# Kernel tuning notes

Hardware: AMD Instinct MI355X
Metric: run time of the kernel (lower is better)

Reference implementation:

```python
import jax, jax.numpy as jnp
import numpy as np

D_K = 64

def setup_inputs() -> dict:
    key = jax.random.key(0)
    kq, kk, kv, km = jax.random.split(key, 4)
    B, H, S, D = 2, 16, 2048, D_K
    q = jax.random.normal(kq, (B, H, S, D), dtype=jnp.float32)
    k = jax.random.normal(kk, (B, H, S, D), dtype=jnp.float32)
    v = jax.random.normal(kv, (B, H, S, D), dtype=jnp.float32)
    atten_mask = jax.random.bernoulli(km, 0.1, (B, H, S, S))  # True = masked out
    return {"q": q, "k": k, "v": v, "atten_mask": atten_mask}

def reference(q, k, v, atten_mask):
    # score = q @ k^T / sqrt(d_k)  -> [B, H, S, S]
    score = jnp.einsum("bhqd,bhkd->bhqk", q, k) / np.sqrt(D_K).astype(np.float32)
    score = jnp.where(atten_mask, jnp.float32(-1e9), score)
    attn = jax.nn.softmax(score, axis=-1)
    return attn  # original module stops before the AV matmul (v unused)
```

## Files before the change

kernel.cpp:

```cpp
#include <hip/hip_runtime.h>

typedef _Float16 f16x8 __attribute__((ext_vector_type(8)));
typedef _Float16 f16x4 __attribute__((ext_vector_type(4)));
typedef float    f32x4 __attribute__((ext_vector_type(4)));
typedef int      i32x4 __attribute__((ext_vector_type(4)));

#define S_LEN 2048
#define D_KH  64
#define NBH   32
#define QTILE 16
#define NBLK  (NBH * (S_LEN / QTILE))
#define THREADS 512
#define QK_ELEMS (NBH * S_LEN * D_KH)

__device__ __forceinline__ f16x8 cvt8(const float4 a, const float4 b) {
  f16x8 r;
  r[0] = (_Float16)a.x; r[1] = (_Float16)a.y;
  r[2] = (_Float16)a.z; r[3] = (_Float16)a.w;
  r[4] = (_Float16)b.x; r[5] = (_Float16)b.y;
  r[6] = (_Float16)b.z; r[7] = (_Float16)b.w;
  return r;
}

__global__ __launch_bounds__(256) void cvt_qk_kernel(
    const float* __restrict__ q, const float* __restrict__ kmat,
    _Float16* __restrict__ qh, _Float16* __restrict__ kh) {
  const long long idx = ((long long)blockIdx.x * 256 + threadIdx.x) * 8;
  float4 q0 = *(const float4*)(q + idx);
  float4 q1 = *(const float4*)(q + idx + 4);
  const float s = 0.125f;
  q0.x *= s; q0.y *= s; q0.z *= s; q0.w *= s;
  q1.x *= s; q1.y *= s; q1.z *= s; q1.w *= s;
  *(f16x8*)(qh + idx) = cvt8(q0, q1);
  const float4 k0 = *(const float4*)(kmat + idx);
  const float4 k1 = *(const float4*)(kmat + idx + 4);
  *(f16x8*)(kh + idx) = cvt8(k0, k1);
}

__device__ __forceinline__ void softmax_row_lds(
    const _Float16* __restrict__ srow, const i32x4* __restrict__ m,
    const int physx, const int l, float* __restrict__ op) {
  float mx = -3.0e38f;
  #pragma unroll
  for (int i = 0; i < 8; ++i) {
    const int col = (i << 8) + (l << 2);
    const f16x4 h = *(const f16x4*)&srow[col ^ physx];
    mx = fmaxf(mx, m[i].x ? -1.0e9f : (float)h[0]);
    mx = fmaxf(mx, m[i].y ? -1.0e9f : (float)h[1]);
    mx = fmaxf(mx, m[i].z ? -1.0e9f : (float)h[2]);
    mx = fmaxf(mx, m[i].w ? -1.0e9f : (float)h[3]);
  }
  #pragma unroll
  for (int off = 32; off > 0; off >>= 1)
    mx = fmaxf(mx, __shfl_xor(mx, off, 64));
  float sum = 0.f;
  #pragma unroll
  for (int i = 0; i < 8; ++i) {
    const int col = (i << 8) + (l << 2);
    const f16x4 h = *(const f16x4*)&srow[col ^ physx];
    sum += __expf((m[i].x ? -1.0e9f : (float)h[0]) - mx);
    sum += __expf((m[i].y ? -1.0e9f : (float)h[1]) - mx);
    sum += __expf((m[i].z ? -1.0e9f : (float)h[2]) - mx);
    sum += __expf((m[i].w ? -1.0e9f : (float)h[3]) - mx);
  }
  #pragma unroll
  for (int off = 32; off > 0; off >>= 1)
    sum += __shfl_xor(sum, off, 64);
  const float inv = 1.0f / sum;
  #pragma unroll
  for (int i = 0; i < 8; ++i) {
    const int col = (i << 8) + (l << 2);
    const f16x4 h = *(const f16x4*)&srow[col ^ physx];
    f32x4 o = { __expf((m[i].x ? -1.0e9f : (float)h[0]) - mx) * inv,
                __expf((m[i].y ? -1.0e9f : (float)h[1]) - mx) * inv,
                __expf((m[i].z ? -1.0e9f : (float)h[2]) - mx) * inv,
                __expf((m[i].w ? -1.0e9f : (float)h[3]) - mx) * inv };
    __builtin_nontemporal_store(o, (f32x4*)(op + col));
  }
}

template <bool F16>
__global__ __launch_bounds__(THREADS, 4) void sdpa_probs_kernel(
    const float* __restrict__ qf, const float* __restrict__ kf,
    const _Float16* __restrict__ qh, const _Float16* __restrict__ kh,
    const int* __restrict__ mask, float* __restrict__ out) {
  const int bid = (int)blockIdx.x;
  const int nb  = (bid & 7) * (NBLK / 8) + (bid >> 3);
  const int bh  = nb >> 7;
  const int qt  = nb & 127;

  __shared__ _Float16 sc[QTILE][S_LEN];

  const int tid   = (int)threadIdx.x;
  const int w     = tid >> 6;
  const int l     = tid & 63;
  const int lo    = l & 15;
  const int g     = l >> 4;
  const int dbase = g << 3;

  const size_t qk_bh = (size_t)bh * S_LEN * D_KH;
  const size_t obh   = (size_t)bh * S_LEN * S_LEN;

  const int rowA = w << 1, rowB = rowA + 1;
  const size_t orowA = obh + (size_t)(qt * QTILE + rowA) * S_LEN;
  const size_t orowB = obh + (size_t)(qt * QTILE + rowB) * S_LEN;

  i32x4 mA[8], mB[8];
  {
    const int* mpA = mask + orowA + (l << 2);
    const int* mpB = mask + orowB + (l << 2);
    #pragma unroll
    for (int i = 0; i < 8; ++i) {
      mA[i] = __builtin_nontemporal_load((const i32x4*)(mpA + (i << 8)));
      mB[i] = __builtin_nontemporal_load((const i32x4*)(mpB + (i << 8)));
    }
  }

  f16x8 a0, a1;
  if constexpr (F16) {
    const _Float16* qp = qh + qk_bh + (size_t)(qt * QTILE + lo) * D_KH + dbase;
    a0 = *(const f16x8*)qp;
    a1 = *(const f16x8*)(qp + 32);
  } else {
    const float* qp = qf + qk_bh + (size_t)(qt * QTILE + lo) * D_KH;
    float4 t0 = *(const float4*)(qp + dbase);
    float4 t1 = *(const float4*)(qp + dbase + 4);
    float4 t2 = *(const float4*)(qp + dbase + 32);
    float4 t3 = *(const float4*)(qp + dbase + 36);
    const float s = 0.125f;
    t0.x *= s; t0.y *= s; t0.z *= s; t0.w *= s;
    t1.x *= s; t1.y *= s; t1.z *= s; t1.w *= s;
    t2.x *= s; t2.y *= s; t2.z *= s; t2.w *= s;
    t3.x *= s; t3.y *= s; t3.z *= s; t3.w *= s;
    a0 = cvt8(t0, t1);
    a1 = cvt8(t2, t3);
  }

  #pragma unroll 2
  for (int kt = 0; kt < 16; ++kt) {
    const int kcol = (w << 8) + (kt << 4) + lo;
    f16x8 b0, b1;
    if constexpr (F16) {
      const _Float16* kp = kh + qk_bh + (size_t)kcol * D_KH + dbase;
      b0 = *(const f16x8*)kp;
      b1 = *(const f16x8*)(kp + 32);
    } else {
      const float* kp = kf + qk_bh + (size_t)kcol * D_KH + dbase;
      b0 = cvt8(*(const float4*)(kp), *(const float4*)(kp + 4));
      b1 = cvt8(*(const float4*)(kp + 32), *(const float4*)(kp + 36));
    }
    f32x4 acc = {0.f, 0.f, 0.f, 0.f};
    acc = __builtin_amdgcn_mfma_f32_16x16x32_f16(a0, b0, acc, 0, 0, 0);
    acc = __builtin_amdgcn_mfma_f32_16x16x32_f16(a1, b1, acc, 0, 0, 0);
    const int phys = kcol ^ (g << 4);
    #pragma unroll
    for (int r = 0; r < 4; ++r)
      sc[(g << 2) + r][phys] = (_Float16)acc[r];
  }

  #pragma unroll
  for (int i = 0; i < 8; ++i) asm volatile("" :: "v"(mA[i]), "v"(mB[i]));
  __syncthreads();

  const int physx = (w >> 1) << 4;
  softmax_row_lds(&sc[rowA][0], mA, physx, l, out + orowA);
  softmax_row_lds(&sc[rowB][0], mB, physx, l, out + orowB);
}

extern "C" void kernel_launch(void* const* d_in, const int* in_sizes, int n_in,
                              void* d_out, int out_size, void* d_ws, size_t ws_size,
                              hipStream_t stream) {
  const float* q    = (const float*)d_in[0];
  const float* kmat = (const float*)d_in[1];
  const int*   mask = (const int*)d_in[3];
  float*       out  = (float*)d_out;

  const size_t need = (size_t)QK_ELEMS * 2 * sizeof(_Float16);
  if (ws_size >= need) {
    _Float16* qh = (_Float16*)d_ws;
    _Float16* kh = qh + QK_ELEMS;
    cvt_qk_kernel<<<dim3(QK_ELEMS / 8 / 256), dim3(256), 0, stream>>>(q, kmat, qh, kh);
    sdpa_probs_kernel<true><<<dim3(NBLK), dim3(THREADS), 0, stream>>>(
        nullptr, nullptr, qh, kh, mask, out);
  } else {
    sdpa_probs_kernel<false><<<dim3(NBLK), dim3(THREADS), 0, stream>>>(
        q, kmat, nullptr, nullptr, mask, out);
  }
}
```

Before: 236.2 us.

## Persistent blocks loop over query tiles, prefetching next tile's mask

The grid shrinks to 512 persistent blocks, each looping over 8 query tiles instead of one tile per block. The mask rows for the next tile are loaded during the current tile's softmax, hiding mask load latency behind compute. The mask is also packed into a 32-bit bitfield per row so fewer registers stay live across the loop. Masked entries now skip the exp. This adds two barriers per tile and reduces the number of blocks available for latency hiding.

New measurement: 399.7 us. +69.2%, slower.

```diff
diff --git a/kernel.cpp b/kernel.cpp
--- a/kernel.cpp
+++ b/kernel.cpp
@@ -9,8 +9,9 @@
 #define D_KH  64
 #define NBH   32
 #define QTILE 16
-#define NBLK  (NBH * (S_LEN / QTILE))
 #define THREADS 512
+#define NBLOCKS 512
+#define NT 8
 #define QK_ELEMS (NBH * S_LEN * D_KH)
 
 __device__ __forceinline__ f16x8 cvt8(const float4 a, const float4 b) {
@@ -37,44 +38,47 @@
   *(f16x8*)(kh + idx) = cvt8(k0, k1);
 }
 
-__device__ __forceinline__ void softmax_row_lds(
-    const _Float16* __restrict__ srow, const i32x4* __restrict__ m,
-    const int physx, const int l, float* __restrict__ op) {
+__device__ __forceinline__ void softmax_row_packed(
+    const _Float16* __restrict__ srow, const unsigned pm, const int physx,
+    const int l, float* __restrict__ op) {
   float mx = -3.0e38f;
+  #pragma unroll
+  for (int i = 0; i < 8; ++i) {
+    const int off = (((i << 8) + (l << 2))) ^ physx;
+    const f16x4 h = *(const f16x4*)&srow[off];
+    const unsigned b = pm >> (4 * i);
+    mx = fmaxf(mx, (b & 1u) ? -1.0e9f : (float)h[0]);
+    mx = fmaxf(mx, (b & 2u) ? -1.0e9f : (float)h[1]);
+    mx = fmaxf(mx, (b & 4u) ? -1.0e9f : (float)h[2]);
+    mx = fmaxf(mx, (b & 8u) ? -1.0e9f : (float)h[3]);
+  }
+  #pragma unroll
+  for (int off = 32; off > 0; off >>= 1)
+    mx = fmaxf(mx, __shfl_xor(mx, off, 64));
+  float sum = 0.f;
+  #pragma unroll
+  for (int i = 0; i < 8; ++i) {
+    const int off = (((i << 8) + (l << 2))) ^ physx;
+    const f16x4 h = *(const f16x4*)&srow[off];
+    const unsigned b = pm >> (4 * i);
+    sum += (b & 1u) ? 0.f : __expf((float)h[0] - mx);
+    sum += (b & 2u) ? 0.f : __expf((float)h[1] - mx);
+    sum += (b & 4u) ? 0.f : __expf((float)h[2] - mx);
+    sum += (b & 8u) ? 0.f : __expf((float)h[3] - mx);
+  }
+  #pragma unroll
+  for (int off = 32; off > 0; off >>= 1)
+    sum += __shfl_xor(sum, off, 64);
+  const float inv = 1.0f / sum;
   #pragma unroll
   for (int i = 0; i < 8; ++i) {
     const int col = (i << 8) + (l << 2);
     const f16x4 h = *(const f16x4*)&srow[col ^ physx];
-    mx = fmaxf(mx, m[i].x ? -1.0e9f : (float)h[0]);
-    mx = fmaxf(mx, m[i].y ? -1.0e9f : (float)h[1]);
-    mx = fmaxf(mx, m[i].z ? -1.0e9f : (float)h[2]);
-    mx = fmaxf(mx, m[i].w ? -1.0e9f : (float)h[3]);
-  }
-  #pragma unroll
-  for (int off = 32; off > 0; off >>= 1)
-    mx = fmaxf(mx, __shfl_xor(mx, off, 64));
-  float sum = 0.f;
-  #pragma unroll
-  for (int i = 0; i < 8; ++i) {
-    const int col = (i << 8) + (l << 2);
-    const f16x4 h = *(const f16x4*)&srow[col ^ physx];
-    sum += __expf((m[i].x ? -1.0e9f : (float)h[0]) - mx);
-    sum += __expf((m[i].y ? -1.0e9f : (float)h[1]) - mx);
-    sum += __expf((m[i].z ? -1.0e9f : (float)h[2]) - mx);
-    sum += __expf((m[i].w ? -1.0e9f : (float)h[3]) - mx);
-  }
-  #pragma unroll
-  for (int off = 32; off > 0; off >>= 1)
-    sum += __shfl_xor(sum, off, 64);
-  const float inv = 1.0f / sum;
-  #pragma unroll
-  for (int i = 0; i < 8; ++i) {
-    const int col = (i << 8) + (l << 2);
-    const f16x4 h = *(const f16x4*)&srow[col ^ physx];
-    f32x4 o = { __expf((m[i].x ? -1.0e9f : (float)h[0]) - mx) * inv,
-                __expf((m[i].y ? -1.0e9f : (float)h[1]) - mx) * inv,
-                __expf((m[i].z ? -1.0e9f : (float)h[2]) - mx) * inv,
-                __expf((m[i].w ? -1.0e9f : (float)h[3]) - mx) * inv };
+    const unsigned b = pm >> (4 * i);
+    f32x4 o = { (b & 1u) ? 0.f : __expf((float)h[0] - mx) * inv,
+                (b & 2u) ? 0.f : __expf((float)h[1] - mx) * inv,
+                (b & 4u) ? 0.f : __expf((float)h[2] - mx) * inv,
+                (b & 8u) ? 0.f : __expf((float)h[3] - mx) * inv };
     __builtin_nontemporal_store(o, (f32x4*)(op + col));
   }
 }
@@ -85,9 +89,9 @@
     const _Float16* __restrict__ qh, const _Float16* __restrict__ kh,
     const int* __restrict__ mask, float* __restrict__ out) {
   const int bid = (int)blockIdx.x;
-  const int nb  = (bid & 7) * (NBLK / 8) + (bid >> 3);
-  const int bh  = nb >> 7;
-  const int qt  = nb & 127;
+  const int nb  = (bid & 7) * (NBLOCKS / 8) + (bid >> 3);
+  const int bh  = nb >> 4;
+  const int jb  = nb & 15;
 
   __shared__ _Float16 sc[QTILE][S_LEN];
 
@@ -101,70 +105,93 @@
   const size_t qk_bh = (size_t)bh * S_LEN * D_KH;
   const size_t obh   = (size_t)bh * S_LEN * S_LEN;
 
-  const int rowA = w << 1, rowB = rowA + 1;
-  const size_t orowA = obh + (size_t)(qt * QTILE + rowA) * S_LEN;
-  const size_t orowB = obh + (size_t)(qt * QTILE + rowB) * S_LEN;
-
-  i32x4 mA[8], mB[8];
-  {
-    const int* mpA = mask + orowA + (l << 2);
-    const int* mpB = mask + orowB + (l << 2);
+  const int rowA = w << 1, rowB = rowA | 1;
+  const int physx = (w >> 1) << 4;
+
+  i32x4 rawA[8], rawB[8];
+
+#define ISSUE_MASKS(qt_) do {                                                  \
+    const int* mpA_ = mask + obh + (size_t)((qt_) * QTILE + rowA) * S_LEN + (l << 2); \
+    const int* mpB_ = mask + obh + (size_t)((qt_) * QTILE + rowB) * S_LEN + (l << 2); \
+    _Pragma("unroll")                                                          \
+    for (int i_ = 0; i_ < 8; ++i_) {                                           \
+      rawA[i_] = __builtin_nontemporal_load((const i32x4*)(mpA_ + (i_ << 8))); \
+      rawB[i_] = __builtin_nontemporal_load((const i32x4*)(mpB_ + (i_ << 8))); \
+    }                                                                          \
+  } while (0)
+
+  ISSUE_MASKS(jb * NT);
+
+  for (int t = 0; t < NT; ++t) {
+    const int qt = jb * NT + t;
+
+    f16x8 a0, a1;
+    if constexpr (F16) {
+      const _Float16* qp = qh + qk_bh + (size_t)(qt * QTILE + lo) * D_KH + dbase;
+      a0 = *(const f16x8*)qp;
+      a1 = *(const f16x8*)(qp + 32);
+    } else {
+      const float* qp = qf + qk_bh + (size_t)(qt * QTILE + lo) * D_KH;
+      float4 t0 = *(const float4*)(qp + dbase);
+      float4 t1 = *(const float4*)(qp + dbase + 4);
+      float4 t2 = *(const float4*)(qp + dbase + 32);
+      float4 t3 = *(const float4*)(qp + dbase + 36);
+      const float s = 0.125f;
+      t0.x *= s; t0.y *= s; t0.z *= s; t0.w *= s;
+      t1.x *= s; t1.y *= s; t1.z *= s; t1.w *= s;
+      t2.x *= s; t2.y *= s; t2.z *= s; t2.w *= s;
+      t3.x *= s; t3.y *= s; t3.z *= s; t3.w *= s;
+      a0 = cvt8(t0, t1);
+      a1 = cvt8(t2, t3);
+    }
+
+    #pragma unroll 2
+    for (int kt = 0; kt < 16; ++kt) {
+      const int kcol = (w << 8) + (kt << 4) + lo;
+      f16x8 b0, b1;
+      if constexpr (F16) {
+        const _Float16* kp = kh + qk_bh + (size_t)kcol * D_KH + dbase;
+        b0 = *(const f16x8*)kp;
+        b1 = *(const f16x8*)(kp + 32);
+      } else {
+        const float* kp = kf + qk_bh + (size_t)kcol * D_KH + dbase;
+        b0 = cvt8(*(const float4*)(kp), *(const float4*)(kp + 4));
+        b1 = cvt8(*(const float4*)(kp + 32), *(const float4*)(kp + 36));
+      }
+      f32x4 acc = {0.f, 0.f, 0.f, 0.f};
+      acc = __builtin_amdgcn_mfma_f32_16x16x32_f16(a0, b0, acc, 0, 0, 0);
+      acc = __builtin_amdgcn_mfma_f32_16x16x32_f16(a1, b1, acc, 0, 0, 0);
+      const int phys = kcol ^ (g << 4);
+      #pragma unroll
+      for (int r = 0; r < 4; ++r)
+        sc[(g << 2) + r][phys] = (_Float16)acc[r];
+    }
+
+    unsigned pA = 0, pB = 0;
     #pragma unroll
     for (int i = 0; i < 8; ++i) {
-      mA[i] = __builtin_nontemporal_load((const i32x4*)(mpA + (i << 8)));
-      mB[i] = __builtin_nontemporal_load((const i32x4*)(mpB + (i << 8)));
+      pA |= ((rawA[i].x != 0 ? 1u : 0u) << (4 * i))
+          | ((rawA[i].y != 0 ? 1u : 0u) << (4 * i + 1))
+          | ((rawA[i].z != 0 ? 1u : 0u) << (4 * i + 2))
+          | ((rawA[i].w != 0 ? 1u : 0u) << (4 * i + 3));
+      pB |= ((rawB[i].x != 0 ? 1u : 0u) << (4 * i))
+          | ((rawB[i].y != 0 ? 1u : 0u) << (4 * i + 1))
+          | ((rawB[i].z != 0 ? 1u : 0u) << (4 * i + 2))
+          | ((rawB[i].w != 0 ? 1u : 0u) << (4 * i + 3));
     }
-  }
-
-  f16x8 a0, a1;
-  if constexpr (F16) {
-    const _Float16* qp = qh + qk_bh + (size_t)(qt * QTILE + lo) * D_KH + dbase;
-    a0 = *(const f16x8*)qp;
-    a1 = *(const f16x8*)(qp + 32);
-  } else {
-    const float* qp = qf + qk_bh + (size_t)(qt * QTILE + lo) * D_KH;
-    float4 t0 = *(const float4*)(qp + dbase);
-    float4 t1 = *(const float4*)(qp + dbase + 4);
-    float4 t2 = *(const float4*)(qp + dbase + 32);
-    float4 t3 = *(const float4*)(qp + dbase + 36);
-    const float s = 0.125f;
-    t0.x *= s; t0.y *= s; t0.z *= s; t0.w *= s;
-    t1.x *= s; t1.y *= s; t1.z *= s; t1.w *= s;
-    t2.x *= s; t2.y *= s; t2.z *= s; t2.w *= s;
-    t3.x *= s; t3.y *= s; t3.z *= s; t3.w *= s;
-    a0 = cvt8(t0, t1);
-    a1 = cvt8(t2, t3);
-  }
-
-  #pragma unroll 2
-  for (int kt = 0; kt < 16; ++kt) {
-    const int kcol = (w << 8) + (kt << 4) + lo;
-    f16x8 b0, b1;
-    if constexpr (F16) {
-      const _Float16* kp = kh + qk_bh + (size_t)kcol * D_KH + dbase;
-      b0 = *(const f16x8*)kp;
-      b1 = *(const f16x8*)(kp + 32);
-    } else {
-      const float* kp = kf + qk_bh + (size_t)kcol * D_KH + dbase;
-      b0 = cvt8(*(const float4*)(kp), *(const float4*)(kp + 4));
-      b1 = cvt8(*(const float4*)(kp + 32), *(const float4*)(kp + 36));
-    }
-    f32x4 acc = {0.f, 0.f, 0.f, 0.f};
-    acc = __builtin_amdgcn_mfma_f32_16x16x32_f16(a0, b0, acc, 0, 0, 0);
-    acc = __builtin_amdgcn_mfma_f32_16x16x32_f16(a1, b1, acc, 0, 0, 0);
-    const int phys = kcol ^ (g << 4);
-    #pragma unroll
-    for (int r = 0; r < 4; ++r)
-      sc[(g << 2) + r][phys] = (_Float16)acc[r];
-  }
-
-  #pragma unroll
-  for (int i = 0; i < 8; ++i) asm volatile("" :: "v"(mA[i]), "v"(mB[i]));
-  __syncthreads();
-
-  const int physx = (w >> 1) << 4;
-  softmax_row_lds(&sc[rowA][0], mA, physx, l, out + orowA);
-  softmax_row_lds(&sc[rowB][0], mB, physx, l, out + orowB);
+
+    if (t + 1 < NT) ISSUE_MASKS(qt + 1);
+
+    __syncthreads();
+
+    const size_t orowA = obh + (size_t)(qt * QTILE + rowA) * S_LEN;
+    const size_t orowB = obh + (size_t)(qt * QTILE + rowB) * S_LEN;
+    softmax_row_packed(&sc[rowA][0], pA, physx, l, out + orowA);
+    softmax_row_packed(&sc[rowB][0], pB, physx, l, out + orowB);
+
+    __syncthreads();
+  }
+#undef ISSUE_MASKS
 }
 
 extern "C" void kernel_launch(void* const* d_in, const int* in_sizes, int n_in,
@@ -180,10 +207,10 @@
     _Float16* qh = (_Float16*)d_ws;
     _Float16* kh = qh + QK_ELEMS;
     cvt_qk_kernel<<<dim3(QK_ELEMS / 8 / 256), dim3(256), 0, stream>>>(q, kmat, qh, kh);
-    sdpa_probs_kernel<true><<<dim3(NBLK), dim3(THREADS), 0, stream>>>(
+    sdpa_probs_kernel<true><<<dim3(NBLOCKS), dim3(THREADS), 0, stream>>>(
         nullptr, nullptr, qh, kh, mask, out);
   } else {
-    sdpa_probs_kernel<false><<<dim3(NBLK), dim3(THREADS), 0, stream>>>(
+    sdpa_probs_kernel<false><<<dim3(NBLOCKS), dim3(THREADS), 0, stream>>>(
         q, kmat, nullptr, nullptr, mask, out);
   }
 }
```
